# Optimization experiments

Hardware: AMD Instinct MI355X
Metric: run time of the kernel (lower is better)

Reference implementation:

```python
import jax, jax.numpy as jnp
import numpy as np
from jax.scipy.ndimage import map_coordinates

N_ANGLES = 120


def _radon3d(vol):
    """Faithful port of radon_transform_3d_pet(axis=2 path) + radon_torch_2d.

    vol: [1, 1, D, H, W].  Slices are vol[:, :, :, d] (dim 3), stacked over
    range(W) -- valid because H == W here.  Returns sinogram stack [S, A, L].
    """
    B, C, D, H, W = vol.shape  # B = C = 1
    imgs = jnp.moveaxis(vol[0, 0], 1, 0)  # [S=H, D, W]; slice s = vol[0,0,:,s,:]

    L = int(np.ceil(np.sqrt(D * D + W * W)))  # padded square canvas
    top = (L - D) // 2   # pad_h // 2
    left = (L - W) // 2  # pad_w // 2

    angles = jnp.linspace(0.0, 120.0, N_ANGLES) * (jnp.pi / 180.0)
    cos_t, sin_t = jnp.cos(angles), jnp.sin(angles)

    # affine_grid with align_corners=True over an L x L output
    lin = jnp.linspace(-1.0, 1.0, L)
    xg, yg = jnp.meshgrid(lin, lin)  # [L, L]; xg varies along columns
    x_in = cos_t[:, None, None] * xg - sin_t[:, None, None] * yg  # [A, L, L]
    y_in = sin_t[:, None, None] * xg + cos_t[:, None, None] * yg
    # unnormalize (align_corners=True) and shift into the UNpadded image frame;
    # zeros in the pad region == map_coordinates mode='constant', cval=0
    ix = (x_in + 1.0) * 0.5 * (L - 1) - left  # column coord into [D, W] image
    iy = (y_in + 1.0) * 0.5 * (L - 1) - top   # row coord

    def sample(im):  # im: [D, W] -> rotated canvases [A, L, L]
        return map_coordinates(im, [iy, ix], order=1, mode='constant', cval=0.0)

    rot = jax.vmap(sample)(imgs)        # [S, A, L, L]
    return rot.sum(axis=2)              # sum over rows -> [S, A, L]


def setup_inputs() -> dict:
    key = jax.random.key(0)
    k1, k2 = jax.random.split(key)
    shape = (1, 1, 64, 64, 64)
    out = jax.random.uniform(k1, shape, dtype=jnp.float32)
    gt = jax.random.uniform(k2, shape, dtype=jnp.float32)
    return {"out": out, "gt": gt}


def reference(out, gt):
    so = _radon3d(out)  # [S, A, L]
    sg = _radon3d(gt)
    # sum over slices of per-slice mean L1 (matches the Python loop of F.l1_loss)
    return jnp.abs(so - sg).mean(axis=(1, 2)).sum()
```

## Files before the change

kernel.cpp:

```cpp
#include <hip/hip_runtime.h>
#include <hip/hip_fp16.h>

#define DD 64
#define NA 120
#define NS 64
#define LL 91
#define PS 67
#define PSTR 69
#define NCELL (PS * PSTR)
#define NSL 4
#define NANG 8
#define JT 96
#define NTHR (NANG * JT)
#define NSP (NS / NSL)
#define NAP (NA / NANG)
#define NBLKS (NSP * NAP)

static __device__ __forceinline__ __half2 u2h(unsigned int u) {
    union { unsigned int u; __half2 h; } v; v.u = u; return v.h;
}
static __device__ __forceinline__ unsigned int h2u(__half2 h) {
    union { __half2 h; unsigned int u; } v; v.h = h; return v.u;
}

__global__ __launch_bounds__(NTHR) void radon_loss_kernel(
    const float* __restrict__ vout, const float* __restrict__ vgt,
    float* __restrict__ out)
{
    __shared__ uint4 C[NCELL];
    __shared__ float wsum[NTHR / 64];

    const int bid = blockIdx.x;
    const int sp = bid / NAP;
    const int ap = bid - sp * NAP;
    const int s0 = sp * NSL;
    const int t = threadIdx.x;

    for (int idx = t; idx < NCELL; idx += NTHR)
        C[idx] = make_uint4(0u, 0u, 0u, 0u);
    __syncthreads();

    for (int idx = t; idx < DD * DD; idx += NTHR) {
        const int d = idx >> 6, w = idx & 63;
        const int g = d * 4096 + s0 * 64 + w;
        const float d0 = vout[g]       - vgt[g];
        const float d1 = vout[g + 64]  - vgt[g + 64];
        const float d2 = vout[g + 128] - vgt[g + 128];
        const float d3 = vout[g + 192] - vgt[g + 192];
        uint2 v8;
        v8.x = h2u(__floats2half2_rn(d0, d1));
        v8.y = h2u(__floats2half2_rn(d2, d3));
        const int rb = (d + 1) * PSTR + w;
        ((uint2*)&C[rb + 1])[0] = v8;
        ((uint2*)&C[rb])[1]     = v8;
    }
    __syncthreads();

    const int ja = t / JT;
    const int j  = t - ja * JT;
    const int a  = ap * NANG + ja;
    const float theta = (float)a * (float)(3.14159265358979323846 * 120.0 / 119.0 / 180.0);
    const float c = cosf(theta), sn = sinf(theta);

    float val = 0.f;
    if (j < LL) {
        const float linj = fmaf((float)j, 2.0f / 90.0f, -1.0f);
        const float bx1 = fmaf(c,  linj, 1.0f) * 45.0f - 12.0f + 45.0f * sn;
        const float by1 = fmaf(sn, linj, 1.0f) * 45.0f - 12.0f - 45.0f * c;
        __half2 acc01 = __floats2half2_rn(0.f, 0.f);
        __half2 acc23 = acc01;
        for (int i = 0; i < LL; ++i) {
            const float xs = fminf(fmaxf(fmaf(-(float)i, sn, bx1), 0.0f), 65.0f);
            const float ys = fminf(fmaxf(fmaf( (float)i, c,  by1), 0.0f), 65.0f);
            const int ix = (int)xs;
            const int iy = (int)ys;
            const float wx = xs - (float)ix;
            const float wy = ys - (float)iy;
            const __half2 wx2 = __float2half2_rn(wx);
            const __half2 wy2 = __float2half2_rn(wy);
            const int ci = iy * PSTR + ix;
            const uint4 q0 = C[ci];
            const uint4 q1 = C[ci + PSTR];
            const __half2 t01 = __hfma2(wx2, __hsub2(u2h(q0.z), u2h(q0.x)), u2h(q0.x));
            const __half2 b01 = __hfma2(wx2, __hsub2(u2h(q1.z), u2h(q1.x)), u2h(q1.x));
            acc01 = __hadd2(acc01, __hfma2(wy2, __hsub2(b01, t01), t01));
            const __half2 t23 = __hfma2(wx2, __hsub2(u2h(q0.w), u2h(q0.y)), u2h(q0.y));
            const __half2 b23 = __hfma2(wx2, __hsub2(u2h(q1.w), u2h(q1.y)), u2h(q1.y));
            acc23 = __hadd2(acc23, __hfma2(wy2, __hsub2(b23, t23), t23));
        }
        const float2 a01 = __half22float2(acc01);
        const float2 a23 = __half22float2(acc23);
        val = fabsf(a01.x) + fabsf(a01.y) + fabsf(a23.x) + fabsf(a23.y);
    }

    #pragma unroll
    for (int off = 32; off > 0; off >>= 1)
        val += __shfl_down(val, off);
    const int wave = t >> 6, lane = t & 63;
    if (lane == 0) wsum[wave] = val;
    __syncthreads();
    if (t == 0) {
        float v = 0.f;
        #pragma unroll
        for (int wv = 0; wv < NTHR / 64; ++wv) v += wsum[wv];
        atomicAdd(out, v * (1.0f / (float)(NA * LL)));
    }
}

extern "C" void kernel_launch(void* const* d_in, const int* in_sizes, int n_in,
                              void* d_out, int out_size, void* d_ws, size_t ws_size,
                              hipStream_t stream) {
    const float* vout = (const float*)d_in[0];
    const float* vgt  = (const float*)d_in[1];
    float* out = (float*)d_out;

    hipMemsetAsync(out, 0, sizeof(float), stream);
    radon_loss_kernel<<<NBLKS, NTHR, 0, stream>>>(vout, vgt, out);
}
```

Before: 77.79 us.

## Store slice differences as FP8 to pack eight slices per LDS cell

Slice differences now go into shared memory as FP8 instead of FP16, so each 16-byte cell holds eight slices rather than four. Each block therefore covers 8 slices and 4 angles, and every gathered cell feeds twice as many accumulations. Interpolation and accumulation move to fp32 using hardware fp8 unpack instructions and precomputed bilinear weights. The inner loop is unrolled and the launch bounds request two blocks per SM. FP8 quantization of the inputs adds numerical error that may exceed the loss tolerance, and the extra unpack instructions add ALU work.

```diff
diff --git a/kernel.cpp b/kernel.cpp
--- a/kernel.cpp
+++ b/kernel.cpp
@@ -1,29 +1,22 @@
 #include <hip/hip_runtime.h>
-#include <hip/hip_fp16.h>
 
 #define DD 64
 #define NA 120
-#define NS 64
 #define LL 91
 #define PS 67
 #define PSTR 69
 #define NCELL (PS * PSTR)
-#define NSL 4
-#define NANG 8
+#define NSL 8
+#define NANG 4
 #define JT 96
 #define NTHR (NANG * JT)
-#define NSP (NS / NSL)
+#define NSP (64 / NSL)
 #define NAP (NA / NANG)
 #define NBLKS (NSP * NAP)
 
-static __device__ __forceinline__ __half2 u2h(unsigned int u) {
-    union { unsigned int u; __half2 h; } v; v.u = u; return v.h;
-}
-static __device__ __forceinline__ unsigned int h2u(__half2 h) {
-    union { __half2 h; unsigned int u; } v; v.h = h; return v.u;
-}
+typedef float f32x2 __attribute__((ext_vector_type(2)));
 
-__global__ __launch_bounds__(NTHR) void radon_loss_kernel(
+__global__ __launch_bounds__(NTHR, 2) void radon_loss_kernel(
     const float* __restrict__ vout, const float* __restrict__ vgt,
     float* __restrict__ out)
 {
@@ -43,16 +36,18 @@
     for (int idx = t; idx < DD * DD; idx += NTHR) {
         const int d = idx >> 6, w = idx & 63;
         const int g = d * 4096 + s0 * 64 + w;
-        const float d0 = vout[g]       - vgt[g];
-        const float d1 = vout[g + 64]  - vgt[g + 64];
-        const float d2 = vout[g + 128] - vgt[g + 128];
-        const float d3 = vout[g + 192] - vgt[g + 192];
-        uint2 v8;
-        v8.x = h2u(__floats2half2_rn(d0, d1));
-        v8.y = h2u(__floats2half2_rn(d2, d3));
+        float df[NSL];
+        #pragma unroll
+        for (int k = 0; k < NSL; ++k)
+            df[k] = vout[g + 64 * k] - vgt[g + 64 * k];
+        int p0 = 0, p1 = 0;
+        p0 = __builtin_amdgcn_cvt_pk_fp8_f32(df[0], df[1], p0, false);
+        p0 = __builtin_amdgcn_cvt_pk_fp8_f32(df[2], df[3], p0, true);
+        p1 = __builtin_amdgcn_cvt_pk_fp8_f32(df[4], df[5], p1, false);
+        p1 = __builtin_amdgcn_cvt_pk_fp8_f32(df[6], df[7], p1, true);
         const int rb = (d + 1) * PSTR + w;
-        ((uint2*)&C[rb + 1])[0] = v8;
-        ((uint2*)&C[rb])[1]     = v8;
+        ((uint2*)&C[rb + 1])[0] = make_uint2((unsigned)p0, (unsigned)p1);
+        ((uint2*)&C[rb])[1]     = make_uint2((unsigned)p0, (unsigned)p1);
     }
     __syncthreads();
 
@@ -67,30 +62,53 @@
         const float linj = fmaf((float)j, 2.0f / 90.0f, -1.0f);
         const float bx1 = fmaf(c,  linj, 1.0f) * 45.0f - 12.0f + 45.0f * sn;
         const float by1 = fmaf(sn, linj, 1.0f) * 45.0f - 12.0f - 45.0f * c;
-        __half2 acc01 = __floats2half2_rn(0.f, 0.f);
-        __half2 acc23 = acc01;
+        float a0 = 0.f, a1 = 0.f, a2 = 0.f, a3 = 0.f;
+        float a4 = 0.f, a5 = 0.f, a6 = 0.f, a7 = 0.f;
+        #pragma unroll 7
         for (int i = 0; i < LL; ++i) {
             const float xs = fminf(fmaxf(fmaf(-(float)i, sn, bx1), 0.0f), 65.0f);
             const float ys = fminf(fmaxf(fmaf( (float)i, c,  by1), 0.0f), 65.0f);
             const int ix = (int)xs;
             const int iy = (int)ys;
-            const float wx = xs - (float)ix;
-            const float wy = ys - (float)iy;
-            const __half2 wx2 = __float2half2_rn(wx);
-            const __half2 wy2 = __float2half2_rn(wy);
+            const float wx = __builtin_amdgcn_fractf(xs);
+            const float wy = __builtin_amdgcn_fractf(ys);
+            const float ux = 1.f - wx, uy = 1.f - wy;
+            const float w00 = ux * uy, w01 = wx * uy;
+            const float w10 = ux * wy, w11 = wx * wy;
             const int ci = iy * PSTR + ix;
             const uint4 q0 = C[ci];
             const uint4 q1 = C[ci + PSTR];
-            const __half2 t01 = __hfma2(wx2, __hsub2(u2h(q0.z), u2h(q0.x)), u2h(q0.x));
-            const __half2 b01 = __hfma2(wx2, __hsub2(u2h(q1.z), u2h(q1.x)), u2h(q1.x));
-            acc01 = __hadd2(acc01, __hfma2(wy2, __hsub2(b01, t01), t01));
-            const __half2 t23 = __hfma2(wx2, __hsub2(u2h(q0.w), u2h(q0.y)), u2h(q0.y));
-            const __half2 b23 = __hfma2(wx2, __hsub2(u2h(q1.w), u2h(q1.y)), u2h(q1.y));
-            acc23 = __hadd2(acc23, __hfma2(wy2, __hsub2(b23, t23), t23));
+            {
+                const f32x2 vA = __builtin_amdgcn_cvt_pk_f32_fp8(q0.x, false);
+                const f32x2 vB = __builtin_amdgcn_cvt_pk_f32_fp8(q0.x, true);
+                const f32x2 vC = __builtin_amdgcn_cvt_pk_f32_fp8(q0.z, false);
+                const f32x2 vD = __builtin_amdgcn_cvt_pk_f32_fp8(q0.z, true);
+                const f32x2 vE = __builtin_amdgcn_cvt_pk_f32_fp8(q1.x, false);
+                const f32x2 vF = __builtin_amdgcn_cvt_pk_f32_fp8(q1.x, true);
+                const f32x2 vG = __builtin_amdgcn_cvt_pk_f32_fp8(q1.z, false);
+                const f32x2 vH = __builtin_amdgcn_cvt_pk_f32_fp8(q1.z, true);
+                a0 = fmaf(w00, vA.x, fmaf(w01, vC.x, fmaf(w10, vE.x, fmaf(w11, vG.x, a0))));
+                a1 = fmaf(w00, vA.y, fmaf(w01, vC.y, fmaf(w10, vE.y, fmaf(w11, vG.y, a1))));
+                a2 = fmaf(w00, vB.x, fmaf(w01, vD.x, fmaf(w10, vF.x, fmaf(w11, vH.x, a2))));
+                a3 = fmaf(w00, vB.y, fmaf(w01, vD.y, fmaf(w10, vF.y, fmaf(w11, vH.y, a3))));
+            }
+            {
+                const f32x2 vA = __builtin_amdgcn_cvt_pk_f32_fp8(q0.y, false);
+                const f32x2 vB = __builtin_amdgcn_cvt_pk_f32_fp8(q0.y, true);
+                const f32x2 vC = __builtin_amdgcn_cvt_pk_f32_fp8(q0.w, false);
+                const f32x2 vD = __builtin_amdgcn_cvt_pk_f32_fp8(q0.w, true);
+                const f32x2 vE = __builtin_amdgcn_cvt_pk_f32_fp8(q1.y, false);
+                const f32x2 vF = __builtin_amdgcn_cvt_pk_f32_fp8(q1.y, true);
+                const f32x2 vG = __builtin_amdgcn_cvt_pk_f32_fp8(q1.w, false);
+                const f32x2 vH = __builtin_amdgcn_cvt_pk_f32_fp8(q1.w, true);
+                a4 = fmaf(w00, vA.x, fmaf(w01, vC.x, fmaf(w10, vE.x, fmaf(w11, vG.x, a4))));
+                a5 = fmaf(w00, vA.y, fmaf(w01, vC.y, fmaf(w10, vE.y, fmaf(w11, vG.y, a5))));
+                a6 = fmaf(w00, vB.x, fmaf(w01, vD.x, fmaf(w10, vF.x, fmaf(w11, vH.x, a6))));
+                a7 = fmaf(w00, vB.y, fmaf(w01, vD.y, fmaf(w10, vF.y, fmaf(w11, vH.y, a7))));
+            }
         }
-        const float2 a01 = __half22float2(acc01);
-        const float2 a23 = __half22float2(acc23);
-        val = fabsf(a01.x) + fabsf(a01.y) + fabsf(a23.x) + fabsf(a23.y);
+        val = fabsf(a0) + fabsf(a1) + fabsf(a2) + fabsf(a3)
+            + fabsf(a4) + fabsf(a5) + fabsf(a6) + fabsf(a7);
     }
 
     #pragma unroll
```

New measurement: 79.84 us. +2.6%, slower.
